# Kernel tuning notes

Measured on AMD Instinct MI355X. Metric: run time of the kernel, lower is better.

Reference implementation:

```python
import jax, jax.numpy as jnp
import numpy as np
from jax import lax

DIM = 192
HEADS = 6
WS = 8
SHIFT = 4
RED = max(8, DIM // 8)  # 24
HID = 4 * DIM


def _rel_index(ws):
    coords = np.stack(np.meshgrid(np.arange(ws), np.arange(ws), indexing='ij'))  # [2,ws,ws]
    flat = coords.reshape(2, -1)
    rel = (flat[:, :, None] - flat[:, None, :]).transpose(1, 2, 0)  # [T,T,2]
    rel[:, :, 0] += ws - 1
    rel[:, :, 1] += ws - 1
    rel[:, :, 0] *= 2 * ws - 1
    return rel.sum(-1)  # [T,T]


def _build_mask(h, w, ws, shift):
    img = np.zeros((h, w))
    slices = (slice(0, -ws), slice(-ws, -shift), slice(-shift, None))
    cnt = 0
    for hs in slices:
        for wcs in slices:
            img[hs, wcs] = cnt
            cnt += 1
    mw = img.reshape(h // ws, ws, w // ws, ws).transpose(0, 2, 1, 3).reshape(-1, ws * ws)
    diff = mw[:, None, :] - mw[:, :, None]  # [nW,T,T], diff[w,i,j]=mw[w,j]-mw[w,i]
    return np.where(diff != 0, -100.0, 0.0).astype(np.float32)


def _ln(x, g, b):
    m = x.mean(-1, keepdims=True)
    v = ((x - m) ** 2).mean(-1, keepdims=True)
    return (x - m) / jnp.sqrt(v + 1e-5) * g + b


def _conv(x, k, b, pad):
    y = lax.conv_general_dilated(x, k, (1, 1), [(pad, pad), (pad, pad)],
                                 dimension_numbers=('NCHW', 'OIHW', 'NCHW'))
    return y + b[None, :, None, None]


def setup_inputs() -> dict:
    key = jax.random.key(0)
    ks = jax.random.split(key, 16)
    rn = lambda k, s, sc=0.02: jax.random.normal(k, s, dtype=jnp.float32) * sc
    C = DIM
    return {
        'x': jax.random.normal(ks[0], (4, 256 * 256, C), dtype=jnp.float32),
        'ln1_g': jnp.ones((C,), jnp.float32), 'ln1_b': jnp.zeros((C,), jnp.float32),
        'w_qkv': rn(ks[1], (3 * C, C)), 'b_qkv': jnp.zeros((3 * C,), jnp.float32),
        'rel_table': rn(ks[2], ((2 * WS - 1) ** 2, HEADS)),
        'w_proj': rn(ks[3], (C, C)), 'b_proj': jnp.zeros((C,), jnp.float32),
        'ln2_g': jnp.ones((C,), jnp.float32), 'ln2_b': jnp.zeros((C,), jnp.float32),
        'w_fc1': rn(ks[4], (HID, C)), 'b_fc1': jnp.zeros((HID,), jnp.float32),
        'w_fc2': rn(ks[5], (C, HID)), 'b_fc2': jnp.zeros((C,), jnp.float32),
        'conv1_w': rn(ks[6], (RED, C, 1, 1)), 'conv1_b': jnp.zeros((RED,), jnp.float32),
        'conv2_w': rn(ks[7], (RED, RED, 3, 3)), 'conv2_b': jnp.zeros((RED,), jnp.float32),
        'conv3_w': rn(ks[8], (C, RED, 1, 1)), 'conv3_b': jnp.zeros((C,), jnp.float32),
        'se_w1': rn(ks[9], (RED, C)), 'se_w2': rn(ks[10], (C, RED)),
        'h': 256, 'w': 256,
    }


def reference(x, ln1_g, ln1_b, w_qkv, b_qkv, rel_table, w_proj, b_proj,
              ln2_g, ln2_b, w_fc1, b_fc1, w_fc2, b_fc2,
              conv1_w, conv1_b, conv2_w, conv2_b, conv3_w, conv3_b,
              se_w1, se_w2, h, w):
    B, _, C = x.shape
    ws, T, nh = WS, WS * WS, HEADS
    hd = C // nh
    scale = hd ** -0.5

    nx = _ln(x, ln1_g, ln1_b).reshape(B, h, w, C)
    local = nx.transpose(0, 3, 1, 2)  # NCHW for LCE

    # shifted window attention
    sh = jnp.roll(nx, (-SHIFT, -SHIFT), axis=(1, 2))
    win = sh.reshape(B, h // ws, ws, w // ws, ws, C).transpose(0, 1, 3, 2, 4, 5).reshape(-1, T, C)
    qkv = (win @ w_qkv.T + b_qkv).reshape(-1, T, 3, nh, hd).transpose(2, 0, 3, 1, 4)
    q, k, v = qkv[0] * scale, qkv[1], qkv[2]  # [BW, nh, T, hd]
    attn = jnp.einsum('whid,whjd->whij', q, k)  # [BW, nh, T, T]
    bias = rel_table[_rel_index(ws).reshape(-1)].reshape(T, T, nh).transpose(2, 0, 1)
    attn = attn + bias[None]
    mask = jnp.asarray(_build_mask(h, w, ws, SHIFT))  # [nW, T, T]
    nW = mask.shape[0]
    attn = attn.reshape(B, nW, nh, T, T) + mask[None, :, None]
    attn = jax.nn.softmax(attn, axis=-1).reshape(-1, nh, T, T)
    out = jnp.einsum('whij,whjd->whid', attn, v).transpose(0, 2, 1, 3).reshape(-1, T, C)
    out = out @ w_proj.T + b_proj
    out = out.reshape(B, h // ws, w // ws, ws, ws, C).transpose(0, 1, 3, 2, 4, 5).reshape(B, h, w, C)
    out = jnp.roll(out, (SHIFT, SHIFT), axis=(1, 2))

    x1 = x + out.reshape(B, h * w, C)
    n2 = _ln(x1, ln2_g, ln2_b)
    mlp = jax.nn.gelu(n2 @ w_fc1.T + b_fc1, approximate=False) @ w_fc2.T + b_fc2
    x2 = x1 + mlp

    # LocalContextExtractor (SE-style)
    y = _conv(local, conv1_w, conv1_b, 0)
    y = _conv(y, conv2_w, conv2_b, 1)
    y = _conv(y, conv3_w, conv3_b, 0)
    y = jnp.where(y >= 0, y, 0.2 * y)  # LeakyReLU(0.2)
    pooled = y.mean(axis=(2, 3))  # [B, C]
    wgt = jax.nn.sigmoid(jax.nn.relu(pooled @ se_w1.T) @ se_w2.T)
    y = y * wgt[:, :, None, None]
    lc = y.reshape(B, C, h * w).transpose(0, 2, 1)
    return x2 + lc
```

## Files before the change

kernel.cpp:

```cpp
#include <hip/hip_runtime.h>
#include <hip/hip_bf16.h>

typedef unsigned short u16;
typedef __attribute__((ext_vector_type(8))) short short8x;
typedef __attribute__((ext_vector_type(4))) float f32x4;
typedef __bf16 bf16x8 __attribute__((ext_vector_type(8)));

#define SCALE 0.17677669529663687f

__device__ __forceinline__ u16 f2bf(float f) {
  unsigned u = __builtin_bit_cast(unsigned, f);
  unsigned r = (u + 0x7FFFu + ((u >> 16) & 1u)) >> 16;
  return (u16)r;
}
__device__ __forceinline__ float bf2f(u16 h) {
  return __builtin_bit_cast(float, ((unsigned)h) << 16);
}
__device__ __forceinline__ float gelu_f(float v) {
  float t = v * v;
  float a = __builtin_fmaf(t, -0.07135481627f, -1.59576912161f);
  float e = __expf(v * a);
  return v * __builtin_amdgcn_rcpf(1.0f + e);
}
__device__ __forceinline__ int swz(int row, int col, int ld) {
  return row * ld + ((((col >> 3) ^ (row & 7)) << 3) | (col & 7));
}
__device__ __forceinline__ short8x ldfrag(const u16* s, int row, int kb, int ld) {
  return *(const short8x*)(s + row * ld + (((kb >> 3) ^ (row & 7)) << 3));
}
__device__ __forceinline__ short8x ldg8(const u16* p) { return *(const short8x*)p; }

__device__ __forceinline__ f32x4 MFMA(short8x a, short8x b, f32x4 c) {
  return __builtin_amdgcn_mfma_f32_16x16x32_bf16(
      __builtin_bit_cast(bf16x8, a), __builtin_bit_cast(bf16x8, b), c, 0, 0, 0);
}

__global__ void cvt_kernel(const float* __restrict__ wqkv, const float* __restrict__ wproj,
                           const float* __restrict__ wfc1, const float* __restrict__ wfc2,
                           const float* __restrict__ c1, const float* __restrict__ c3,
                           const float* __restrict__ c2,
                           u16* oq, u16* op, u16* o1, u16* o2, u16* oc1, u16* oc3,
                           float* ow2r) {
  int i = blockIdx.x * 256 + threadIdx.x;
  if (i < 110592) { float f = wqkv[i]; if (i < 36864) f *= SCALE; oq[i] = f2bf(f); return; }
  i -= 110592;
  if (i < 36864) { op[i] = f2bf(wproj[i]); return; }
  i -= 36864;
  if (i < 147456) { o1[i] = f2bf(wfc1[i]); return; }
  i -= 147456;
  if (i < 147456) { o2[i] = f2bf(wfc2[i]); return; }
  i -= 147456;
  if (i < 6144) { int r = i / 192, c = i - r * 192; oc1[i] = (r < 24) ? f2bf(c1[r * 192 + c]) : (u16)0; return; }
  i -= 6144;
  if (i < 6144) { int cc = i >> 5, k = i & 31; oc3[i] = (k < 24) ? f2bf(c3[cc * 24 + k]) : (u16)0; return; }
  i -= 6144;
  if (i < 5184) { int t = i / 576, rr = i - t * 576; int ci = rr / 24, co = rr - ci * 24;
                  ow2r[i] = c2[co * 216 + ci * 9 + t]; }
}

__global__ __launch_bounds__(256) void ln1_kernel(const float* __restrict__ x,
                                                  const float* __restrict__ g,
                                                  const float* __restrict__ b,
                                                  u16* __restrict__ nx) {
  const int wid = threadIdx.x >> 6, lane = threadIdx.x & 63;
  const int row = blockIdx.x * 4 + wid;
  const float* xr = x + row * 192;
  float v0 = xr[lane], v1 = xr[lane + 64], v2 = xr[lane + 128];
  float s = v0 + v1 + v2;
  for (int m = 1; m < 64; m <<= 1) s += __shfl_xor(s, m);
  const float mean = s * (1.0f / 192.0f);
  const float d0 = v0 - mean, d1 = v1 - mean, d2 = v2 - mean;
  float q = d0 * d0 + d1 * d1 + d2 * d2;
  for (int m = 1; m < 64; m <<= 1) q += __shfl_xor(q, m);
  const float rstd = rsqrtf(q * (1.0f / 192.0f) + 1e-5f);
  u16* o = nx + row * 192;
  o[lane]       = f2bf(d0 * rstd * g[lane] + b[lane]);
  o[lane + 64]  = f2bf(d1 * rstd * g[lane + 64] + b[lane + 64]);
  o[lane + 128] = f2bf(d2 * rstd * g[lane + 128] + b[lane + 128]);
}

__global__ __launch_bounds__(768, 3) void attn_kernel(
    const float* __restrict__ x, const u16* __restrict__ nx,
    const u16* __restrict__ wq, const float* __restrict__ bqkv,
    const float* __restrict__ rel, const u16* __restrict__ wp,
    const float* __restrict__ bproj, float* __restrict__ x1out) {
  __shared__ u16 sU[6 * 64 * 64];
  __shared__ u16 sQKV[64 * 576];
  __shared__ float sRel[225 * 6];
  __shared__ int sG[64];

  const int tid = threadIdx.x, blk = blockIdx.x;
  const int b = blk >> 10, wi = (blk >> 5) & 31, wj = blk & 31;
  const int wv = tid >> 6, lane = tid & 63, lr = lane & 15, hi = lane >> 4;

  for (int i = tid; i < 1350; i += 768) sRel[i] = rel[i];
  if (tid < 64) {
    int si = (wi * 8 + (tid >> 3) + 4) & 255, sj = (wj * 8 + (tid & 7) + 4) & 255;
    sG[tid] = b * 65536 + si * 256 + sj;
  }
  for (int i = tid; i < 64 * 96; i += 768) {
    int r = i / 96, w32 = i - r * 96;
    int si = (wi * 8 + (r >> 3) + 4) & 255, sj = (wj * 8 + (r & 7) + 4) & 255;
    int grow = b * 65536 + si * 256 + sj;
    unsigned v = ((const unsigned*)nx)[grow * 96 + w32];
    ((unsigned*)sU)[r * 96 + ((((w32 >> 2) ^ (r & 7)) << 2) | (w32 & 3))] = v;
  }
  __syncthreads();

  for (int nt0 = 0; nt0 < 3; ++nt0) {
    const int ocol = (wv * 3 + nt0) * 16 + lr;
    short8x Bf[6];
#pragma unroll
    for (int kk = 0; kk < 6; ++kk) Bf[kk] = ldg8(wq + ocol * 192 + kk * 32 + hi * 8);
    const float bias = bqkv[ocol] * (ocol < 192 ? SCALE : 1.0f);
#pragma unroll
    for (int mt = 0; mt < 4; ++mt) {
      f32x4 acc = {0.f, 0.f, 0.f, 0.f};
#pragma unroll
      for (int kk = 0; kk < 6; ++kk)
        acc = MFMA(ldfrag(sU, mt * 16 + lr, kk * 32 + hi * 8, 192), Bf[kk], acc);
#pragma unroll
      for (int r = 0; r < 4; ++r)
        sQKV[swz(mt * 16 + hi * 4 + r, ocol, 576)] = f2bf(acc[r] + bias);
    }
  }
  __syncthreads();

  const int h = wv >> 1, half = wv & 1;
  {
    short8x Aq[2], Bk[4];
#pragma unroll
    for (int i2 = 0; i2 < 2; ++i2)
      Aq[i2] = ldfrag(sQKV, (half * 2 + i2) * 16 + lr, h * 32 + hi * 8, 576);
#pragma unroll
    for (int t4 = 0; t4 < 4; ++t4)
      Bk[t4] = ldfrag(sQKV, t4 * 16 + lr, 192 + h * 32 + hi * 8, 576);
    f32x4 S[2][4];
#pragma unroll
    for (int i2 = 0; i2 < 2; ++i2)
#pragma unroll
      for (int nt = 0; nt < 4; ++nt)
        S[i2][nt] = MFMA(Aq[i2], Bk[nt], (f32x4){0.f, 0.f, 0.f, 0.f});

#pragma unroll
    for (int i2 = 0; i2 < 2; ++i2)
#pragma unroll
      for (int r = 0; r < 4; ++r) {
        const int tI = (half * 2 + i2) * 16 + hi * 4 + r;
        const int tri = tI >> 3, trj = tI & 7;
        const int ui = wi * 8 + tri, vi = wj * 8 + trj;
        const int rgi = (ui >= 248) + (ui >= 252), cgi = (vi >= 248) + (vi >= 252);
#pragma unroll
        for (int nt = 0; nt < 4; ++nt) {
          const int tJ = nt * 16 + lr;
          const int tci = tJ >> 3, tcj = tJ & 7;
          const int idx = (tri - tci + 7) * 15 + (trj - tcj + 7);
          float v = S[i2][nt][r] + sRel[idx * 6 + h];
          const int uj = wi * 8 + tci, vj = wj * 8 + tcj;
          const int rgj = (uj >= 248) + (uj >= 252), cgj = (vj >= 248) + (vj >= 252);
          if ((rgi != rgj) | (cgi != cgj)) v -= 100.0f;
          S[i2][nt][r] = v;
        }
      }
#pragma unroll
    for (int i2 = 0; i2 < 2; ++i2)
#pragma unroll
      for (int r = 0; r < 4; ++r) {
        float mx = fmaxf(fmaxf(S[i2][0][r], S[i2][1][r]), fmaxf(S[i2][2][r], S[i2][3][r]));
        mx = fmaxf(mx, __shfl_xor(mx, 1));
        mx = fmaxf(mx, __shfl_xor(mx, 2));
        mx = fmaxf(mx, __shfl_xor(mx, 4));
        mx = fmaxf(mx, __shfl_xor(mx, 8));
        float sm = 0.f;
#pragma unroll
        for (int nt = 0; nt < 4; ++nt) { float e = __expf(S[i2][nt][r] - mx); S[i2][nt][r] = e; sm += e; }
        sm += __shfl_xor(sm, 1); sm += __shfl_xor(sm, 2);
        sm += __shfl_xor(sm, 4); sm += __shfl_xor(sm, 8);
        const float inv = 1.0f / sm;
        const int row = (half * 2 + i2) * 16 + hi * 4 + r;
#pragma unroll
        for (int nt = 0; nt < 4; ++nt)
          sU[h * 4096 + swz(row, nt * 16 + lr, 64)] = f2bf(S[i2][nt][r] * inv);
      }
  }
  __syncthreads();

  {
    const u16* Ph = sU + h * 4096;
    const int nt = half;
    const int dcol = 384 + h * 32 + nt * 16 + lr;
    f32x4 o[4] = {{0.f,0.f,0.f,0.f},{0.f,0.f,0.f,0.f},{0.f,0.f,0.f,0.f},{0.f,0.f,0.f,0.f}};
#pragma unroll
    for (int kk = 0; kk < 2; ++kk) {
      short8x Bv;
#pragma unroll
      for (int jj = 0; jj < 8; ++jj)
        Bv[jj] = (short)sQKV[swz(kk * 32 + hi * 8 + jj, dcol, 576)];
#pragma unroll
      for (int mt = 0; mt < 4; ++mt)
        o[mt] = MFMA(ldfrag(Ph, mt * 16 + lr, kk * 32 + hi * 8, 64), Bv, o[mt]);
    }
    __syncthreads();
#pragma unroll
    for (int mt = 0; mt < 4; ++mt)
#pragma unroll
      for (int r = 0; r < 4; ++r)
        sQKV[swz(mt * 16 + hi * 4 + r, h * 32 + nt * 16 + lr, 576)] = f2bf(o[mt][r]);
  }
  __syncthreads();

  {
    const int ocol = wv * 16 + lr;
    short8x Bf[6];
#pragma unroll
    for (int kk = 0; kk < 6; ++kk) Bf[kk] = ldg8(wp + ocol * 192 + kk * 32 + hi * 8);
    const float bb = bproj[ocol];
#pragma unroll
    for (int mt = 0; mt < 4; ++mt) {
      f32x4 acc = {0.f, 0.f, 0.f, 0.f};
#pragma unroll
      for (int kk = 0; kk < 6; ++kk)
        acc = MFMA(ldfrag(sQKV, mt * 16 + lr, kk * 32 + hi * 8, 576), Bf[kk], acc);
#pragma unroll
      for (int r = 0; r < 4; ++r) {
        const int grow = sG[mt * 16 + hi * 4 + r];
        x1out[grow * 192 + ocol] = x[grow * 192 + ocol] + acc[r] + bb;
      }
    }
  }
}

__global__ __launch_bounds__(256) void conv1_kernel(const u16* __restrict__ nx,
                                                    const u16* __restrict__ w1,
                                                    const float* __restrict__ b1,
                                                    float* __restrict__ y1) {
  const int tid = threadIdx.x, wv = tid >> 6, lane = tid & 63, lr = lane & 15, hi = lane >> 4;
  const int g0 = blockIdx.x * 64;
  const int mt = wv;
  short8x Af[6];
#pragma unroll
  for (int kk = 0; kk < 6; ++kk)
    Af[kk] = ldg8(nx + (g0 + mt * 16 + lr) * 192 + kk * 32 + hi * 8);
  const int bI = g0 >> 16;
  const int hw0 = g0 & 65535;
#pragma unroll
  for (int nt = 0; nt < 2; ++nt) {
    f32x4 acc = {0.f, 0.f, 0.f, 0.f};
#pragma unroll
    for (int kk = 0; kk < 6; ++kk) {
      short8x Bf = ldg8(w1 + (nt * 16 + lr) * 192 + kk * 32 + hi * 8);
      acc = MFMA(Af[kk], Bf, acc);
    }
    const int c = nt * 16 + lr;
    if (c < 24) {
      const float bb = b1[c];
#pragma unroll
      for (int r = 0; r < 4; ++r) {
        const int pix = hw0 + mt * 16 + hi * 4 + r;
        y1[(bI * 24 + c) * 65536 + pix] = acc[r] + bb;
      }
    }
  }
}

__global__ __launch_bounds__(256) void conv2_kernel(const float* __restrict__ y1,
                                                    const float* __restrict__ w2r,
                                                    const float* __restrict__ cb2,
                                                    u16* __restrict__ y2) {
  const int j = threadIdx.x;
  const int i = blockIdx.x & 255;
  const int b = blockIdx.x >> 8;
  float acc[24];
#pragma unroll
  for (int r = 0; r < 24; ++r) acc[r] = cb2[r];
  const float* base = y1 + b * 24 * 65536;
  for (int t = 0; t < 9; ++t) {
    const int dh = t / 3 - 1, dw = t % 3 - 1;
    const int ii = i + dh, jj = j + dw;
    const bool ok = (ii >= 0) & (ii < 256) & (jj >= 0) & (jj < 256);
    const int offc = ok ? (ii * 256 + jj) : 0;
    const float* wt = w2r + t * 576;
    float v[24];
#pragma unroll
    for (int ci = 0; ci < 24; ++ci) {
      float vv = base[ci * 65536 + offc];
      v[ci] = ok ? vv : 0.0f;
    }
#pragma unroll
    for (int ci = 0; ci < 24; ++ci)
#pragma unroll
      for (int co = 0; co < 24; ++co)
        acc[co] += v[ci] * wt[ci * 24 + co];
  }
  u16* o = y2 + (b * 65536 + i * 256 + j) * 32;
#pragma unroll
  for (int r = 0; r < 24; ++r) o[r] = f2bf(acc[r]);
  ((unsigned long long*)(o + 24))[0] = 0ull;
  ((unsigned long long*)(o + 24))[1] = 0ull;
}

__global__ __launch_bounds__(256) void conv3_kernel(const u16* __restrict__ y2,
                                                    const u16* __restrict__ w3,
                                                    const float* __restrict__ b3,
                                                    u16* __restrict__ y,
                                                    float* __restrict__ pooled) {
  const int tid = threadIdx.x, wv = tid >> 6, lane = tid & 63, lr = lane & 15, hi = lane >> 4;
  const int g0 = blockIdx.x * 64;
  short8x Af[4];
#pragma unroll
  for (int mt = 0; mt < 4; ++mt)
    Af[mt] = ldg8(y2 + (g0 + mt * 16 + lr) * 32 + hi * 8);
  const int bI = g0 >> 16;
#pragma unroll
  for (int nt0 = 0; nt0 < 3; ++nt0) {
    const int c = (wv * 3 + nt0) * 16 + lr;
    short8x Bf = ldg8(w3 + c * 32 + hi * 8);
    const float bb = b3[c];
    float colsum = 0.f;
#pragma unroll
    for (int mt = 0; mt < 4; ++mt) {
      f32x4 acc = {0.f, 0.f, 0.f, 0.f};
      acc = MFMA(Af[mt], Bf, acc);
#pragma unroll
      for (int r = 0; r < 4; ++r) {
        float v = acc[r] + bb;
        v = (v >= 0.f) ? v : 0.2f * v;
        y[(g0 + mt * 16 + hi * 4 + r) * 192 + c] = f2bf(v);
        colsum += v;
      }
    }
    colsum += __shfl_xor(colsum, 16);
    colsum += __shfl_xor(colsum, 32);
    if (hi == 0) atomicAdd(&pooled[bI * 192 + c], colsum);
  }
}

__global__ void se_kernel(const float* __restrict__ pooled, const float* __restrict__ w1,
                          const float* __restrict__ w2, float* __restrict__ wgt) {
  __shared__ float t[24];
  const int b = blockIdx.x, lane = threadIdx.x;
  if (lane < 24) {
    float s = 0.f;
    for (int c = 0; c < 192; ++c) s += pooled[b * 192 + c] * (1.0f / 65536.0f) * w1[lane * 192 + c];
    t[lane] = fmaxf(s, 0.0f);
  }
  __syncthreads();
  for (int c = lane; c < 192; c += 64) {
    float s = 0.f;
#pragma unroll
    for (int r = 0; r < 24; ++r) s += t[r] * w2[c * 24 + r];
    wgt[b * 192 + c] = 1.0f / (1.0f + __expf(-s));
  }
}

__global__ __launch_bounds__(768, 6) void mlp_kernel(
    const float* x1, const float* __restrict__ g2, const float* __restrict__ b2,
    const u16* __restrict__ w1m, const float* __restrict__ bf1,
    const u16* __restrict__ w2m, const float* __restrict__ bf2,
    const u16* __restrict__ y, const float* __restrict__ wgt, float* out) {
  __shared__ u16 sN[64 * 192];
  __shared__ u16 sH[64 * 192];
  const int tid = threadIdx.x, wv = tid >> 6, lane = tid & 63, lr = lane & 15, hi = lane >> 4;
  const int g0 = blockIdx.x * 64;

  for (int row = wv; row < 64; row += 12) {
    const float* xr = x1 + (g0 + row) * 192;
    float v0 = xr[lane], v1 = xr[lane + 64], v2 = xr[lane + 128];
    float s = v0 + v1 + v2;
    for (int m = 1; m < 64; m <<= 1) s += __shfl_xor(s, m);
    const float mean = s * (1.0f / 192.0f);
    const float d0 = v0 - mean, d1 = v1 - mean, d2 = v2 - mean;
    float q = d0 * d0 + d1 * d1 + d2 * d2;
    for (int m = 1; m < 64; m <<= 1) q += __shfl_xor(q, m);
    const float rstd = rsqrtf(q * (1.0f / 192.0f) + 1e-5f);
    sN[swz(row, lane, 192)]       = f2bf(d0 * rstd * g2[lane] + b2[lane]);
    sN[swz(row, lane + 64, 192)]  = f2bf(d1 * rstd * g2[lane + 64] + b2[lane + 64]);
    sN[swz(row, lane + 128, 192)] = f2bf(d2 * rstd * g2[lane + 128] + b2[lane + 128]);
  }
  __syncthreads();

  f32x4 acc[4] = {};
  for (int c = 0; c < 4; ++c) {
    const int hcol = c * 192 + wv * 16 + lr;
    f32x4 a1[4] = {};
#pragma unroll
    for (int kk = 0; kk < 6; ++kk) {
      short8x B = ldg8(w1m + hcol * 192 + kk * 32 + hi * 8);
#pragma unroll
      for (int mt = 0; mt < 4; ++mt)
        a1[mt] = MFMA(ldfrag(sN, mt * 16 + lr, kk * 32 + hi * 8, 192), B, a1[mt]);
    }
    if (c) __syncthreads();
    const float bb1 = bf1[hcol];
#pragma unroll
    for (int mt = 0; mt < 4; ++mt)
#pragma unroll
      for (int r = 0; r < 4; ++r)
        sH[swz(mt * 16 + hi * 4 + r, wv * 16 + lr, 192)] = f2bf(gelu_f(a1[mt][r] + bb1));
    __syncthreads();
#pragma unroll
    for (int kk = 0; kk < 6; ++kk) {
      short8x B = ldg8(w2m + (wv * 16 + lr) * 768 + c * 192 + kk * 32 + hi * 8);
#pragma unroll
      for (int mt = 0; mt < 4; ++mt)
        acc[mt] = MFMA(ldfrag(sH, mt * 16 + lr, kk * 32 + hi * 8, 192), B, acc[mt]);
    }
  }

  const int bI = g0 >> 16;
  const int ocol = wv * 16 + lr;
  const float bb = bf2[ocol];
  const float wg = wgt[bI * 192 + ocol];
#pragma unroll
  for (int mt = 0; mt < 4; ++mt)
#pragma unroll
    for (int r = 0; r < 4; ++r) {
      const int grow = g0 + mt * 16 + hi * 4 + r;
      const float lc = bf2f(y[grow * 192 + ocol]) * wg;
      out[grow * 192 + ocol] = x1[grow * 192 + ocol] + acc[mt][r] + bb + lc;
    }
}

extern "C" void kernel_launch(void* const* d_in, const int* in_sizes, int n_in,
                              void* d_out, int out_size, void* d_ws, size_t ws_size,
                              hipStream_t stream) {
  const float* x     = (const float*)d_in[0];
  const float* ln1g  = (const float*)d_in[1];
  const float* ln1b  = (const float*)d_in[2];
  const float* wqkv  = (const float*)d_in[3];
  const float* bqkv  = (const float*)d_in[4];
  const float* rel   = (const float*)d_in[5];
  const float* wproj = (const float*)d_in[6];
  const float* bproj = (const float*)d_in[7];
  const float* ln2g  = (const float*)d_in[8];
  const float* ln2b  = (const float*)d_in[9];
  const float* wfc1  = (const float*)d_in[10];
  const float* bfc1  = (const float*)d_in[11];
  const float* wfc2  = (const float*)d_in[12];
  const float* bfc2  = (const float*)d_in[13];
  const float* c1w   = (const float*)d_in[14];
  const float* c1b   = (const float*)d_in[15];
  const float* c2w   = (const float*)d_in[16];
  const float* c2b   = (const float*)d_in[17];
  const float* c3w   = (const float*)d_in[18];
  const float* c3b   = (const float*)d_in[19];
  const float* sew1  = (const float*)d_in[20];
  const float* sew2  = (const float*)d_in[21];

  char* ws = (char*)d_ws;
  u16*   nx   = (u16*)(ws + 0);
  float* y1   = (float*)(ws + 100663296);
  u16*   y2   = (u16*)(ws + 125829120);
  u16*   yb   = (u16*)(ws + 142606336);
  u16*   wq   = (u16*)(ws + 243269632);
  u16*   wp   = (u16*)(ws + 243490816);
  u16*   w1m  = (u16*)(ws + 243564544);
  u16*   w2m  = (u16*)(ws + 243859456);
  u16*   cw1  = (u16*)(ws + 244154368);
  u16*   cw3  = (u16*)(ws + 244166656);
  float* w2r  = (float*)(ws + 244178944);
  float* pool = (float*)(ws + 244199680);
  float* wgt  = (float*)(ws + 244202752);
  float* out  = (float*)d_out;

  hipMemsetAsync(pool, 0, 3072, stream);
  cvt_kernel<<<1797, 256, 0, stream>>>(wqkv, wproj, wfc1, wfc2, c1w, c3w, c2w,
                                       wq, wp, w1m, w2m, cw1, cw3, w2r);
  ln1_kernel<<<65536, 256, 0, stream>>>(x, ln1g, ln1b, nx);
  attn_kernel<<<4096, 768, 0, stream>>>(x, nx, wq, bqkv, rel, wp, bproj, out);
  conv1_kernel<<<4096, 256, 0, stream>>>(nx, cw1, c1b, y1);
  conv2_kernel<<<1024, 256, 0, stream>>>(y1, w2r, c2b, y2);
  conv3_kernel<<<4096, 256, 0, stream>>>(y2, cw3, c3b, yb, pool);
  se_kernel<<<4, 64, 0, stream>>>(pool, sew1, sew2, wgt);
  mlp_kernel<<<4096, 768, 0, stream>>>(out, ln2g, ln2b, w1m, bfc1, w2m, bfc2, yb, wgt, out);
}
```

Baseline: 1.024 ms.

## Widen per-wave MFMA tiles in MLP, store V transposed in attention

The MLP kernel moves from 12 to 4 waves per block, and each wave now computes three 16-column output tiles, so every LDS A-fragment load feeds three MFMAs. The QKV projection in the attention kernel is restructured the same way, and V is written transposed into its own shared buffer. This lets the PV product load V fragments with a vectorized ldfrag instead of eight scalar LDS reads, and removes one barrier. The cost is higher register pressure and fewer waves per block, which may reduce latency hiding; the launch-bound occupancy hints are also dropped.

```diff
diff --git a/kernel.cpp b/kernel.cpp
--- a/kernel.cpp
+++ b/kernel.cpp
@@ -79,13 +79,14 @@
   o[lane + 128] = f2bf(d2 * rstd * g[lane + 128] + b[lane + 128]);
 }
 
-__global__ __launch_bounds__(768, 3) void attn_kernel(
+__global__ __launch_bounds__(768) void attn_kernel(
     const float* __restrict__ x, const u16* __restrict__ nx,
     const u16* __restrict__ wq, const float* __restrict__ bqkv,
     const float* __restrict__ rel, const u16* __restrict__ wp,
     const float* __restrict__ bproj, float* __restrict__ x1out) {
   __shared__ u16 sU[6 * 64 * 64];
-  __shared__ u16 sQKV[64 * 576];
+  __shared__ u16 sQK[64 * 384];
+  __shared__ u16 sVT[192 * 64];
   __shared__ float sRel[225 * 6];
   __shared__ int sG[64];
 
@@ -107,21 +108,42 @@
   }
   __syncthreads();
 
-  for (int nt0 = 0; nt0 < 3; ++nt0) {
-    const int ocol = (wv * 3 + nt0) * 16 + lr;
-    short8x Bf[6];
-#pragma unroll
-    for (int kk = 0; kk < 6; ++kk) Bf[kk] = ldg8(wq + ocol * 192 + kk * 32 + hi * 8);
-    const float bias = bqkv[ocol] * (ocol < 192 ? SCALE : 1.0f);
+  {
+    const int base = wv * 48;
+    short8x Bf[3][6];
+#pragma unroll
+    for (int j = 0; j < 3; ++j)
+#pragma unroll
+      for (int kk = 0; kk < 6; ++kk)
+        Bf[j][kk] = ldg8(wq + (base + j * 16 + lr) * 192 + kk * 32 + hi * 8);
+    float bias[3];
+#pragma unroll
+    for (int j = 0; j < 3; ++j) {
+      const int ocol = base + j * 16 + lr;
+      bias[j] = bqkv[ocol] * (ocol < 192 ? SCALE : 1.0f);
+    }
 #pragma unroll
     for (int mt = 0; mt < 4; ++mt) {
-      f32x4 acc = {0.f, 0.f, 0.f, 0.f};
-#pragma unroll
-      for (int kk = 0; kk < 6; ++kk)
-        acc = MFMA(ldfrag(sU, mt * 16 + lr, kk * 32 + hi * 8, 192), Bf[kk], acc);
-#pragma unroll
-      for (int r = 0; r < 4; ++r)
-        sQKV[swz(mt * 16 + hi * 4 + r, ocol, 576)] = f2bf(acc[r] + bias);
+      f32x4 aa[3] = {};
+#pragma unroll
+      for (int kk = 0; kk < 6; ++kk) {
+        short8x A = ldfrag(sU, mt * 16 + lr, kk * 32 + hi * 8, 192);
+#pragma unroll
+        for (int j = 0; j < 3; ++j) aa[j] = MFMA(A, Bf[j][kk], aa[j]);
+      }
+      if (wv < 8) {
+#pragma unroll
+        for (int j = 0; j < 3; ++j)
+#pragma unroll
+          for (int r = 0; r < 4; ++r)
+            sQK[swz(mt * 16 + hi * 4 + r, base + j * 16 + lr, 384)] = f2bf(aa[j][r] + bias[j]);
+      } else {
+#pragma unroll
+        for (int j = 0; j < 3; ++j)
+#pragma unroll
+          for (int r = 0; r < 4; ++r)
+            sVT[swz(base - 384 + j * 16 + lr, mt * 16 + hi * 4 + r, 64)] = f2bf(aa[j][r] + bias[j]);
+      }
     }
   }
   __syncthreads();
@@ -131,10 +153,10 @@
     short8x Aq[2], Bk[4];
 #pragma unroll
     for (int i2 = 0; i2 < 2; ++i2)
-      Aq[i2] = ldfrag(sQKV, (half * 2 + i2) * 16 + lr, h * 32 + hi * 8, 576);
+      Aq[i2] = ldfrag(sQK, (half * 2 + i2) * 16 + lr, h * 32 + hi * 8, 384);
 #pragma unroll
     for (int t4 = 0; t4 < 4; ++t4)
-      Bk[t4] = ldfrag(sQKV, t4 * 16 + lr, 192 + h * 32 + hi * 8, 576);
+      Bk[t4] = ldfrag(sQK, t4 * 16 + lr, 192 + h * 32 + hi * 8, 384);
     f32x4 S[2][4];
 #pragma unroll
     for (int i2 = 0; i2 < 2; ++i2)
@@ -188,24 +210,19 @@
   {
     const u16* Ph = sU + h * 4096;
     const int nt = half;
-    const int dcol = 384 + h * 32 + nt * 16 + lr;
-    f32x4 o[4] = {{0.f,0.f,0.f,0.f},{0.f,0.f,0.f,0.f},{0.f,0.f,0.f,0.f},{0.f,0.f,0.f,0.f}};
+    f32x4 o[4] = {};
 #pragma unroll
     for (int kk = 0; kk < 2; ++kk) {
-      short8x Bv;
-#pragma unroll
-      for (int jj = 0; jj < 8; ++jj)
-        Bv[jj] = (short)sQKV[swz(kk * 32 + hi * 8 + jj, dcol, 576)];
+      short8x Bv = ldfrag(sVT, h * 32 + nt * 16 + lr, kk * 32 + hi * 8, 64);
 #pragma unroll
       for (int mt = 0; mt < 4; ++mt)
         o[mt] = MFMA(ldfrag(Ph, mt * 16 + lr, kk * 32 + hi * 8, 64), Bv, o[mt]);
     }
-    __syncthreads();
 #pragma unroll
     for (int mt = 0; mt < 4; ++mt)
 #pragma unroll
       for (int r = 0; r < 4; ++r)
-        sQKV[swz(mt * 16 + hi * 4 + r, h * 32 + nt * 16 + lr, 576)] = f2bf(o[mt][r]);
+        sQK[swz(mt * 16 + hi * 4 + r, h * 32 + nt * 16 + lr, 384)] = f2bf(o[mt][r]);
   }
   __syncthreads();
 
@@ -220,7 +237,7 @@
       f32x4 acc = {0.f, 0.f, 0.f, 0.f};
 #pragma unroll
       for (int kk = 0; kk < 6; ++kk)
-        acc = MFMA(ldfrag(sQKV, mt * 16 + lr, kk * 32 + hi * 8, 576), Bf[kk], acc);
+        acc = MFMA(ldfrag(sQK, mt * 16 + lr, kk * 32 + hi * 8, 384), Bf[kk], acc);
 #pragma unroll
       for (int r = 0; r < 4; ++r) {
         const int grow = sG[mt * 16 + hi * 4 + r];
@@ -353,7 +370,7 @@
   }
 }
 
-__global__ __launch_bounds__(768, 6) void mlp_kernel(
+__global__ __launch_bounds__(256) void mlp_kernel(
     const float* x1, const float* __restrict__ g2, const float* __restrict__ b2,
     const u16* __restrict__ w1m, const float* __restrict__ bf1,
     const u16* __restrict__ w2m, const float* __restrict__ bf2,
@@ -363,7 +380,7 @@
   const int tid = threadIdx.x, wv = tid >> 6, lane = tid & 63, lr = lane & 15, hi = lane >> 4;
   const int g0 = blockIdx.x * 64;
 
-  for (int row = wv; row < 64; row += 12) {
+  for (int row = wv; row < 64; row += 4) {
     const float* xr = x1 + (g0 + row) * 192;
     float v0 = xr[lane], v1 = xr[lane + 64], v2 = xr[lane + 128];
     float s = v0 + v1 + v2;
@@ -379,46 +396,64 @@
   }
   __syncthreads();
 
-  f32x4 acc[4] = {};
+  f32x4 acc[4][3] = {};
   for (int c = 0; c < 4; ++c) {
-    const int hcol = c * 192 + wv * 16 + lr;
-    f32x4 a1[4] = {};
+    f32x4 a1[4][3] = {};
 #pragma unroll
     for (int kk = 0; kk < 6; ++kk) {
-      short8x B = ldg8(w1m + hcol * 192 + kk * 32 + hi * 8);
+      short8x B0 = ldg8(w1m + (c * 192 + wv * 48 + lr) * 192 + kk * 32 + hi * 8);
+      short8x B1 = ldg8(w1m + (c * 192 + wv * 48 + 16 + lr) * 192 + kk * 32 + hi * 8);
+      short8x B2 = ldg8(w1m + (c * 192 + wv * 48 + 32 + lr) * 192 + kk * 32 + hi * 8);
+#pragma unroll
+      for (int mt = 0; mt < 4; ++mt) {
+        short8x A = ldfrag(sN, mt * 16 + lr, kk * 32 + hi * 8, 192);
+        a1[mt][0] = MFMA(A, B0, a1[mt][0]);
+        a1[mt][1] = MFMA(A, B1, a1[mt][1]);
+        a1[mt][2] = MFMA(A, B2, a1[mt][2]);
+      }
+    }
+    if (c) __syncthreads();
+#pragma unroll
+    for (int nt = 0; nt < 3; ++nt) {
+      const float bb1 = bf1[c * 192 + wv * 48 + nt * 16 + lr];
 #pragma unroll
       for (int mt = 0; mt < 4; ++mt)
-        a1[mt] = MFMA(ldfrag(sN, mt * 16 + lr, kk * 32 + hi * 8, 192), B, a1[mt]);
-    }
-    if (c) __syncthreads();
-    const float bb1 = bf1[hcol];
+#pragma unroll
+        for (int r = 0; r < 4; ++r)
+          sH[swz(mt * 16 + hi * 4 + r, wv * 48 + nt * 16 + lr, 192)] =
+              f2bf(gelu_f(a1[mt][nt][r] + bb1));
+    }
+    __syncthreads();
+#pragma unroll
+    for (int kk = 0; kk < 6; ++kk) {
+      short8x B0 = ldg8(w2m + (wv * 48 + lr) * 768 + c * 192 + kk * 32 + hi * 8);
+      short8x B1 = ldg8(w2m + (wv * 48 + 16 + lr) * 768 + c * 192 + kk * 32 + hi * 8);
+      short8x B2 = ldg8(w2m + (wv * 48 + 32 + lr) * 768 + c * 192 + kk * 32 + hi * 8);
+#pragma unroll
+      for (int mt = 0; mt < 4; ++mt) {
+        short8x A = ldfrag(sH, mt * 16 + lr, kk * 32 + hi * 8, 192);
+        acc[mt][0] = MFMA(A, B0, acc[mt][0]);
+        acc[mt][1] = MFMA(A, B1, acc[mt][1]);
+        acc[mt][2] = MFMA(A, B2, acc[mt][2]);
+      }
+    }
+  }
+
+  const int bI = g0 >> 16;
+#pragma unroll
+  for (int nt = 0; nt < 3; ++nt) {
+    const int ocol = wv * 48 + nt * 16 + lr;
+    const float bb = bf2[ocol];
+    const float wg = wgt[bI * 192 + ocol];
 #pragma unroll
     for (int mt = 0; mt < 4; ++mt)
 #pragma unroll
-      for (int r = 0; r < 4; ++r)
-        sH[swz(mt * 16 + hi * 4 + r, wv * 16 + lr, 192)] = f2bf(gelu_f(a1[mt][r] + bb1));
-    __syncthreads();
-#pragma unroll
-    for (int kk = 0; kk < 6; ++kk) {
-      short8x B = ldg8(w2m + (wv * 16 + lr) * 768 + c * 192 + kk * 32 + hi * 8);
-#pragma unroll
-      for (int mt = 0; mt < 4; ++mt)
-        acc[mt] = MFMA(ldfrag(sH, mt * 16 + lr, kk * 32 + hi * 8, 192), B, acc[mt]);
-    }
-  }
-
-  const int bI = g0 >> 16;
-  const int ocol = wv * 16 + lr;
-  const float bb = bf2[ocol];
-  const float wg = wgt[bI * 192 + ocol];
-#pragma unroll
-  for (int mt = 0; mt < 4; ++mt)
-#pragma unroll
-    for (int r = 0; r < 4; ++r) {
-      const int grow = g0 + mt * 16 + hi * 4 + r;
-      const float lc = bf2f(y[grow * 192 + ocol]) * wg;
-      out[grow * 192 + ocol] = x1[grow * 192 + ocol] + acc[mt][r] + bb + lc;
-    }
+      for (int r = 0; r < 4; ++r) {
+        const int grow = g0 + mt * 16 + hi * 4 + r;
+        const float lc = bf2f(y[grow * 192 + ocol]) * wg;
+        out[grow * 192 + ocol] = x1[grow * 192 + ocol] + acc[mt][nt][r] + bb + lc;
+      }
+  }
 }
 
 extern "C" void kernel_launch(void* const* d_in, const int* in_sizes, int n_in,
@@ -472,5 +507,5 @@
   conv2_kernel<<<1024, 256, 0, stream>>>(y1, w2r, c2b, y2);
   conv3_kernel<<<4096, 256, 0, stream>>>(y2, cw3, c3b, yb, pool);
   se_kernel<<<4, 64, 0, stream>>>(pool, sew1, sew2, wgt);
-  mlp_kernel<<<4096, 768, 0, stream>>>(out, ln2g, ln2b, w1m, bfc1, w2m, bfc2, yb, wgt, out);
-}
+  mlp_kernel<<<4096, 256, 0, stream>>>(out, ln2g, ln2b, w1m, bfc1, w2m, bfc2, yb, wgt, out);
+}
```

Result: slower. 1.170 ms (+14.3%).
